# Kernel tuning notes

Measured on AMD Instinct MI355X. Metric: run time of the kernel, lower is better.

## Reference

```python
import jax, jax.numpy as jnp
import numpy as np

B, L, D = 64, 512, 768

def setup_inputs() -> dict:
    key = jax.random.key(0)
    k1, k2, k3, k4 = jax.random.split(key, 4)
    hidden_states = jax.random.normal(k1, (B, L, D), dtype=jnp.float32)
    # nn.Linear(hidden_size, hidden_size): weight [D, D], bias [D]
    W = jax.random.normal(k2, (D, D), dtype=jnp.float32) * (1.0 / np.sqrt(D))
    b = jax.random.normal(k3, (D,), dtype=jnp.float32) * 0.02
    # context_vector: [D, 1]
    context_vector = jax.random.normal(k4, (D, 1), dtype=jnp.float32)
    return {"hidden_states": hidden_states, "W": W, "b": b, "context_vector": context_vector}

def reference(hidden_states, W, b, context_vector):
    # tanh(dense(h)): [B, L, D]; torch Linear uses x @ W.T + b
    proj = jnp.tanh(jnp.einsum('bld,ed->ble', hidden_states, W) + b)
    # scores: [B, L]
    scores = jnp.einsum('bld,d->bl', proj, context_vector[:, 0])
    # softmax over sequence dim (dim=1)
    attention_weights = jax.nn.softmax(scores, axis=1)
    # weighted sum over sequence: [B, D]
    weighted_output = jnp.einsum('bld,bl->bd', hidden_states, attention_weights)
    return (weighted_output, attention_weights)
```

## Files before the change

### kernel.cpp

```cpp
#include <hip/hip_runtime.h>
#include <hip/hip_bf16.h>


using half8 = __attribute__((ext_vector_type(8))) _Float16;
using f32x4 = __attribute__((ext_vector_type(4))) float;

#define AS1 __attribute__((address_space(1)))
#define AS3 __attribute__((address_space(3)))

__device__ __forceinline__ void gload_lds16(const void* g, void* l) {
  __builtin_amdgcn_global_load_lds((const AS1 void*)g, (AS3 void*)l, 16, 0, 0);
}

__device__ __forceinline__ unsigned short f2h(float x) {
  _Float16 h = (_Float16)x;
  return __builtin_bit_cast(unsigned short, h);
}

__device__ __forceinline__ float tanh_fast(float x) {
  return 1.0f - __fdividef(2.0f, 1.0f + __expf(2.0f * x));
}


__global__ void convert_h(const float4* __restrict__ H4, ushort4* __restrict__ Ah) {
  int i = blockIdx.x * 256 + threadIdx.x;
  float4 x = H4[i];
  ushort4 o;
  o.x = f2h(x.x); o.y = f2h(x.y); o.z = f2h(x.z); o.w = f2h(x.w);
  Ah[i] = o;
}

__global__ void convert_w(const float4* __restrict__ W4, ushort4* __restrict__ Wt) {
  int i = blockIdx.x * 256 + threadIdx.x;
  float4 x = W4[i];
  ushort4 o;
  o.x = f2h(x.x); o.y = f2h(x.y); o.z = f2h(x.z); o.w = f2h(x.w);
  Wt[i] = o;
}


__device__ __forceinline__ void stage_tiles(const char* abase, const char* bbase,
                                            char* ldsAbuf, char* ldsBbuf, int tid) {
  char* ldsAw = ldsAbuf + ((tid >> 6) << 10);
  char* ldsBw = ldsBbuf + ((tid >> 6) << 10);
  #pragma unroll
  for (int r = 0; r < 4; ++r) {
    int off = tid * 16 + r * 4096;
    int row = off >> 7;
    int col = (off & 127) ^ ((row & 7) << 4);
    gload_lds16(abase + row * 1536 + col, ldsAw + r * 4096);
  }
  #pragma unroll
  for (int r = 0; r < 4; ++r) {
    int off = tid * 16 + r * 4096;
    int row = off >> 7;
    int col = (off & 127) ^ ((row & 7) << 4);
    gload_lds16(bbase + row * 1536 + col, ldsBw + r * 4096);
  }
}

__device__ __forceinline__ void compute_tile(const ushort* ldsAbuf, const ushort* ldsBbuf,
                                             int wr, int wc, int m, int q,
                                             f32x4 acc[4][4]) {
  #pragma unroll
  for (int ks = 0; ks < 2; ++ks) {
    half8 areg[4], breg[4];
    #pragma unroll
    for (int mi = 0; mi < 4; ++mi) {
      int row = wr * 64 + mi * 16 + m;
      int col = (ks * 64 + q * 16) ^ ((row & 7) << 4);
      areg[mi] = *(const half8*)((const char*)ldsAbuf + row * 128 + col);
    }
    #pragma unroll
    for (int ni = 0; ni < 4; ++ni) {
      int row = wc * 64 + ni * 16 + m;
      int col = (ks * 64 + q * 16) ^ ((row & 7) << 4);
      breg[ni] = *(const half8*)((const char*)ldsBbuf + row * 128 + col);
    }
    #pragma unroll
    for (int mi = 0; mi < 4; ++mi)
      #pragma unroll
      for (int ni = 0; ni < 4; ++ni)
        acc[mi][ni] = __builtin_amdgcn_mfma_f32_16x16x32_f16(
            areg[mi], breg[ni], acc[mi][ni], 0, 0, 0);
  }
}

__global__ __launch_bounds__(256) void gemm_scores(
    const ushort* __restrict__ Ah, const ushort* __restrict__ Wt,
    const float* __restrict__ bias, const float* __restrict__ cvec,
    float* __restrict__ part) {
  __shared__ ushort ldsA[2][8192];
  __shared__ ushort ldsB[2][8192];
  __shared__ float scpart[2][128];

  const int tid = threadIdx.x;
  const int lane = tid & 63;
  const int wid = tid >> 6;
  const int wr = wid >> 1, wc = wid & 1;
  const int m = lane & 15, q = lane >> 4;

  const int bid = blockIdx.x;
  const int xcd = bid & 7;
  const int slot = bid >> 3;
  const int mtile = xcd * 32 + slot / 6;
  const int ntile = slot % 6;

  f32x4 acc[4][4];
  #pragma unroll
  for (int a = 0; a < 4; ++a)
    #pragma unroll
    for (int b2 = 0; b2 < 4; ++b2)
      acc[a][b2] = (f32x4){0.f, 0.f, 0.f, 0.f};

  const char* const abase0 = (const char*)Ah + (size_t)(mtile * 128) * 1536;
  const char* const bbase0 = (const char*)Wt + (size_t)(ntile * 128) * 1536;

  stage_tiles(abase0, bbase0, (char*)ldsA[0], (char*)ldsB[0], tid);
  __syncthreads();

  #pragma unroll
  for (int kb2 = 0; kb2 < 6; ++kb2) {
    stage_tiles(abase0 + (kb2 * 2 + 1) * 128, bbase0 + (kb2 * 2 + 1) * 128,
                (char*)ldsA[1], (char*)ldsB[1], tid);
    compute_tile(ldsA[0], ldsB[0], wr, wc, m, q, acc);
    __syncthreads();

    if (kb2 < 5)
      stage_tiles(abase0 + (kb2 * 2 + 2) * 128, bbase0 + (kb2 * 2 + 2) * 128,
                  (char*)ldsA[0], (char*)ldsB[0], tid);
    compute_tile(ldsA[1], ldsB[1], wr, wc, m, q, acc);
    __syncthreads();
  }

  float bb[4], cc[4];
  #pragma unroll
  for (int ni = 0; ni < 4; ++ni) {
    int e = ntile * 128 + wc * 64 + ni * 16 + m;
    bb[ni] = bias[e];
    cc[ni] = cvec[e];
  }
  #pragma unroll
  for (int mi = 0; mi < 4; ++mi) {
    #pragma unroll
    for (int j = 0; j < 4; ++j) {
      float s = 0.f;
      #pragma unroll
      for (int ni = 0; ni < 4; ++ni)
        s += tanh_fast(acc[mi][ni][j] + bb[ni]) * cc[ni];
      s += __shfl_xor(s, 1);
      s += __shfl_xor(s, 2);
      s += __shfl_xor(s, 4);
      s += __shfl_xor(s, 8);
      if (m == 0) scpart[wc][wr * 64 + mi * 16 + q * 4 + j] = s;
    }
  }
  __syncthreads();
  if (tid < 128)
    part[ntile * 32768 + mtile * 128 + tid] = scpart[0][tid] + scpart[1][tid];
}

__global__ void softmax_k(const float* __restrict__ part, float* __restrict__ attn) {
  int b = blockIdx.x, l = threadIdx.x;
  int r = b * 512 + l;
  float s = part[r] + part[32768 + r] + part[2 * 32768 + r] +
            part[3 * 32768 + r] + part[4 * 32768 + r] + part[5 * 32768 + r];
  __shared__ float redm[8], reds[8];
  float mx = s;
  #pragma unroll
  for (int o = 32; o >= 1; o >>= 1) mx = fmaxf(mx, __shfl_xor(mx, o));
  if ((l & 63) == 0) redm[l >> 6] = mx;
  __syncthreads();
  mx = redm[0];
  #pragma unroll
  for (int i = 1; i < 8; ++i) mx = fmaxf(mx, redm[i]);
  float e = expf(s - mx);
  float sm = e;
  #pragma unroll
  for (int o = 32; o >= 1; o >>= 1) sm += __shfl_xor(sm, o);
  if ((l & 63) == 0) reds[l >> 6] = sm;
  __syncthreads();
  float tot = reds[0];
  #pragma unroll
  for (int i = 1; i < 8; ++i) tot += reds[i];
  attn[r] = e / tot;
}

__global__ void wsum_k(const ushort* __restrict__ Ah, const float* __restrict__ attn,
                       float* __restrict__ out) {
  int b = blockIdx.x, dc = blockIdx.y;
  int t = threadIdx.x;
  __shared__ float w[512];
  #pragma unroll
  for (int i = 0; i < 4; ++i) w[t + i * 128] = attn[b * 512 + t + i * 128];
  __syncthreads();
  int d0 = dc * 256 + t * 2;
  const ushort* hp = Ah + (size_t)b * 512 * 768 + d0;
  float a0 = 0.f, a1 = 0.f;
  #pragma unroll 8
  for (int l = 0; l < 512; ++l) {
    unsigned u = *(const unsigned*)(hp + (size_t)l * 768);
    float wl = w[l];
    a0 += wl * (float)__builtin_bit_cast(_Float16, (unsigned short)(u & 0xffff));
    a1 += wl * (float)__builtin_bit_cast(_Float16, (unsigned short)(u >> 16));
  }
  out[b * 768 + d0] = a0;
  out[b * 768 + d0 + 1] = a1;
}

extern "C" void kernel_launch(void* const* d_in, const int* in_sizes, int n_in,
                              void* d_out, int out_size, void* d_ws, size_t ws_size,
                              hipStream_t stream) {
  const float* H    = (const float*)d_in[0];
  const float* W    = (const float*)d_in[1];
  const float* bias = (const float*)d_in[2];
  const float* cvec = (const float*)d_in[3];
  float* out = (float*)d_out;

  char* ws = (char*)d_ws;
  ushort* Ah = (ushort*)(ws + 0);
  ushort* Wt = (ushort*)(ws + 50331648);
  float*  prt = (float*)(ws + 51511296);

  hipLaunchKernelGGL(convert_h, dim3(24576), dim3(256), 0, stream,
                     (const float4*)H, (ushort4*)Ah);
  hipLaunchKernelGGL(convert_w, dim3(576), dim3(256), 0, stream,
                     (const float4*)W, (ushort4*)Wt);
  hipLaunchKernelGGL(gemm_scores, dim3(1536), dim3(256), 0, stream,
                     Ah, Wt, bias, cvec, prt);
  hipLaunchKernelGGL(softmax_k, dim3(64), dim3(512), 0, stream, prt, out + 49152);
  hipLaunchKernelGGL(wsum_k, dim3(64, 3), dim3(128), 0, stream,
                     Ah, out + 49152, out);
}
```

Before: 112.6 us.

## Halve GEMM K-tile to raise occupancy and fuse softmax into weighted sum

```diff
diff --git a/kernel.cpp b/kernel.cpp
--- a/kernel.cpp
+++ b/kernel.cpp
@@ -39,59 +39,56 @@
 }
 
 
-__device__ __forceinline__ void stage_tiles(const char* abase, const char* bbase,
-                                            char* ldsAbuf, char* ldsBbuf, int tid) {
+__device__ __forceinline__ void stage_tiles32(const char* abase, const char* bbase,
+                                              char* ldsAbuf, char* ldsBbuf, int tid) {
   char* ldsAw = ldsAbuf + ((tid >> 6) << 10);
   char* ldsBw = ldsBbuf + ((tid >> 6) << 10);
   #pragma unroll
-  for (int r = 0; r < 4; ++r) {
+  for (int r = 0; r < 2; ++r) {
     int off = tid * 16 + r * 4096;
-    int row = off >> 7;
-    int col = (off & 127) ^ ((row & 7) << 4);
+    int row = off >> 6;
+    int col = (off & 63) ^ ((row & 3) << 4);
     gload_lds16(abase + row * 1536 + col, ldsAw + r * 4096);
   }
   #pragma unroll
-  for (int r = 0; r < 4; ++r) {
+  for (int r = 0; r < 2; ++r) {
     int off = tid * 16 + r * 4096;
-    int row = off >> 7;
-    int col = (off & 127) ^ ((row & 7) << 4);
+    int row = off >> 6;
+    int col = (off & 63) ^ ((row & 3) << 4);
     gload_lds16(bbase + row * 1536 + col, ldsBw + r * 4096);
   }
 }
 
-__device__ __forceinline__ void compute_tile(const ushort* ldsAbuf, const ushort* ldsBbuf,
-                                             int wr, int wc, int m, int q,
-                                             f32x4 acc[4][4]) {
-  #pragma unroll
-  for (int ks = 0; ks < 2; ++ks) {
-    half8 areg[4], breg[4];
-    #pragma unroll
-    for (int mi = 0; mi < 4; ++mi) {
-      int row = wr * 64 + mi * 16 + m;
-      int col = (ks * 64 + q * 16) ^ ((row & 7) << 4);
-      areg[mi] = *(const half8*)((const char*)ldsAbuf + row * 128 + col);
-    }
-    #pragma unroll
-    for (int ni = 0; ni < 4; ++ni) {
-      int row = wc * 64 + ni * 16 + m;
-      int col = (ks * 64 + q * 16) ^ ((row & 7) << 4);
-      breg[ni] = *(const half8*)((const char*)ldsBbuf + row * 128 + col);
-    }
-    #pragma unroll
-    for (int mi = 0; mi < 4; ++mi)
-      #pragma unroll
-      for (int ni = 0; ni < 4; ++ni)
-        acc[mi][ni] = __builtin_amdgcn_mfma_f32_16x16x32_f16(
-            areg[mi], breg[ni], acc[mi][ni], 0, 0, 0);
-  }
-}
-
-__global__ __launch_bounds__(256) void gemm_scores(
+__device__ __forceinline__ void compute_tile32(const ushort* ldsAbuf, const ushort* ldsBbuf,
+                                               int wr, int wc, int m, int q,
+                                               f32x4 acc[4][4]) {
+  half8 areg[4], breg[4];
+  #pragma unroll
+  for (int mi = 0; mi < 4; ++mi) {
+    int row = wr * 64 + mi * 16 + m;
+    int col = (q * 16) ^ ((row & 3) << 4);
+    areg[mi] = *(const half8*)((const char*)ldsAbuf + row * 64 + col);
+  }
+  #pragma unroll
+  for (int ni = 0; ni < 4; ++ni) {
+    int row = wc * 64 + ni * 16 + m;
+    int col = (q * 16) ^ ((row & 3) << 4);
+    breg[ni] = *(const half8*)((const char*)ldsBbuf + row * 64 + col);
+  }
+  #pragma unroll
+  for (int mi = 0; mi < 4; ++mi)
+    #pragma unroll
+    for (int ni = 0; ni < 4; ++ni)
+      acc[mi][ni] = __builtin_amdgcn_mfma_f32_16x16x32_f16(
+          areg[mi], breg[ni], acc[mi][ni], 0, 0, 0);
+}
+
+__global__ __launch_bounds__(256, 4) void gemm_scores(
     const ushort* __restrict__ Ah, const ushort* __restrict__ Wt,
     const float* __restrict__ bias, const float* __restrict__ cvec,
     float* __restrict__ part) {
-  __shared__ ushort ldsA[2][8192];
-  __shared__ ushort ldsB[2][8192];
+  __shared__ ushort ldsA[2][4096];
+  __shared__ ushort ldsB[2][4096];
   __shared__ float scpart[2][128];
 
   const int tid = threadIdx.x;
@@ -116,20 +113,20 @@
   const char* const abase0 = (const char*)Ah + (size_t)(mtile * 128) * 1536;
   const char* const bbase0 = (const char*)Wt + (size_t)(ntile * 128) * 1536;
 
-  stage_tiles(abase0, bbase0, (char*)ldsA[0], (char*)ldsB[0], tid);
-  __syncthreads();
-
-  #pragma unroll
-  for (int kb2 = 0; kb2 < 6; ++kb2) {
-    stage_tiles(abase0 + (kb2 * 2 + 1) * 128, bbase0 + (kb2 * 2 + 1) * 128,
-                (char*)ldsA[1], (char*)ldsB[1], tid);
-    compute_tile(ldsA[0], ldsB[0], wr, wc, m, q, acc);
+  stage_tiles32(abase0, bbase0, (char*)ldsA[0], (char*)ldsB[0], tid);
+  __syncthreads();
+
+  #pragma unroll
+  for (int kb2 = 0; kb2 < 12; ++kb2) {
+    stage_tiles32(abase0 + (kb2 * 2 + 1) * 64, bbase0 + (kb2 * 2 + 1) * 64,
+                  (char*)ldsA[1], (char*)ldsB[1], tid);
+    compute_tile32(ldsA[0], ldsB[0], wr, wc, m, q, acc);
     __syncthreads();
 
-    if (kb2 < 5)
-      stage_tiles(abase0 + (kb2 * 2 + 2) * 128, bbase0 + (kb2 * 2 + 2) * 128,
-                  (char*)ldsA[0], (char*)ldsB[0], tid);
-    compute_tile(ldsA[1], ldsB[1], wr, wc, m, q, acc);
+    if (kb2 < 11)
+      stage_tiles32(abase0 + (kb2 * 2 + 2) * 64, bbase0 + (kb2 * 2 + 2) * 64,
+                    (char*)ldsA[0], (char*)ldsB[0], tid);
+    compute_tile32(ldsA[1], ldsB[1], wr, wc, m, q, acc);
     __syncthreads();
   }
 
@@ -160,40 +157,39 @@
     part[ntile * 32768 + mtile * 128 + tid] = scpart[0][tid] + scpart[1][tid];
 }
 
-__global__ void softmax_k(const float* __restrict__ part, float* __restrict__ attn) {
-  int b = blockIdx.x, l = threadIdx.x;
-  int r = b * 512 + l;
-  float s = part[r] + part[32768 + r] + part[2 * 32768 + r] +
-            part[3 * 32768 + r] + part[4 * 32768 + r] + part[5 * 32768 + r];
-  __shared__ float redm[8], reds[8];
-  float mx = s;
-  #pragma unroll
-  for (int o = 32; o >= 1; o >>= 1) mx = fmaxf(mx, __shfl_xor(mx, o));
-  if ((l & 63) == 0) redm[l >> 6] = mx;
-  __syncthreads();
-  mx = redm[0];
-  #pragma unroll
-  for (int i = 1; i < 8; ++i) mx = fmaxf(mx, redm[i]);
-  float e = expf(s - mx);
-  float sm = e;
-  #pragma unroll
-  for (int o = 32; o >= 1; o >>= 1) sm += __shfl_xor(sm, o);
-  if ((l & 63) == 0) reds[l >> 6] = sm;
-  __syncthreads();
-  float tot = reds[0];
-  #pragma unroll
-  for (int i = 1; i < 8; ++i) tot += reds[i];
-  attn[r] = e / tot;
-}
-
-__global__ void wsum_k(const ushort* __restrict__ Ah, const float* __restrict__ attn,
-                       float* __restrict__ out) {
+__global__ void wsum_fused(const ushort* __restrict__ Ah, const float* __restrict__ prt,
+                           float* __restrict__ out) {
   int b = blockIdx.x, dc = blockIdx.y;
   int t = threadIdx.x;
   __shared__ float w[512];
-  #pragma unroll
-  for (int i = 0; i < 4; ++i) w[t + i * 128] = attn[b * 512 + t + i * 128];
-  __syncthreads();
+  __shared__ float redm[2], reds[2];
+
+  float s[4];
+  #pragma unroll
+  for (int i = 0; i < 4; ++i) {
+    int r = b * 512 + t + i * 128;
+    s[i] = prt[r] + prt[32768 + r] + prt[2 * 32768 + r] +
+           prt[3 * 32768 + r] + prt[4 * 32768 + r] + prt[5 * 32768 + r];
+  }
+  float mx = fmaxf(fmaxf(s[0], s[1]), fmaxf(s[2], s[3]));
+  #pragma unroll
+  for (int o = 32; o >= 1; o >>= 1) mx = fmaxf(mx, __shfl_xor(mx, o));
+  if ((t & 63) == 0) redm[t >> 6] = mx;
+  __syncthreads();
+  mx = fmaxf(redm[0], redm[1]);
+
+  float e[4], sm = 0.f;
+  #pragma unroll
+  for (int i = 0; i < 4; ++i) { e[i] = __expf(s[i] - mx); sm += e[i]; }
+  #pragma unroll
+  for (int o = 32; o >= 1; o >>= 1) sm += __shfl_xor(sm, o);
+  if ((t & 63) == 0) reds[t >> 6] = sm;
+  __syncthreads();
+  float inv = 1.0f / (reds[0] + reds[1]);
+  #pragma unroll
+  for (int i = 0; i < 4; ++i) w[t + i * 128] = e[i] * inv;
+  __syncthreads();
+
   int d0 = dc * 256 + t * 2;
   const ushort* hp = Ah + (size_t)b * 512 * 768 + d0;
   float a0 = 0.f, a1 = 0.f;
@@ -206,6 +202,12 @@
   }
   out[b * 768 + d0] = a0;
   out[b * 768 + d0 + 1] = a1;
+
+  if (dc == 0) {
+    #pragma unroll
+    for (int i = 0; i < 4; ++i)
+      out[49152 + b * 512 + t + i * 128] = w[t + i * 128];
+  }
 }
 
 extern "C" void kernel_launch(void* const* d_in, const int* in_sizes, int n_in,
@@ -228,7 +230,6 @@
                      (const float4*)W, (ushort4*)Wt);
   hipLaunchKernelGGL(gemm_scores, dim3(1536), dim3(256), 0, stream,
                      Ah, Wt, bias, cvec, prt);
-  hipLaunchKernelGGL(softmax_k, dim3(64), dim3(512), 0, stream, prt, out + 49152);
-  hipLaunchKernelGGL(wsum_k, dim3(64, 3), dim3(128), 0, stream,
-                     Ah, out + 49152, out);
-}
+  hipLaunchKernelGGL(wsum_fused, dim3(64, 3), dim3(128), 0, stream,
+                     Ah, prt, out);
+}
```

After: 117.0 us. 1.04x slower.
